# Optimization experiments

Hardware: AMD Instinct MI355X
Metric: run time of the kernel (lower is better)

The kernel has to match this reference:

```python
import jax, jax.numpy as jnp
import numpy as np

B, N, M, HA, HB, H = 16, 256, 12, 64, 64, 4
DIN = 2 * HA + HB
DOUT = 4 * H * HA


def _bn(x, g, b, eps=1e-5):
    # BatchNorm1d forward with batch statistics (training-mode math), x: [R, C]
    m = jnp.mean(x, axis=0)
    v = jnp.var(x, axis=0)
    return (x - m) * jax.lax.rsqrt(v + eps) * g + b


def setup_inputs() -> dict:
    key = jax.random.key(0)
    ks = jax.random.split(key, 6)
    atom_emb = jax.random.normal(ks[0], (B, N, HA), jnp.float32)
    nbr_emb = jax.random.normal(ks[1], (B, N, M, HB), jnp.float32)
    nbr_adj_list = jax.random.randint(ks[2], (B, N, M), 0, N)
    atom_mask = jnp.ones((B, N, 1), jnp.float32)
    W_full = jax.random.normal(ks[3], (DIN, DOUT), jnp.float32) / np.sqrt(DIN)
    b_full = jnp.zeros((DOUT,), jnp.float32)
    W_final = jax.random.normal(ks[4], (H * HA, HA), jnp.float32) / np.sqrt(H * HA)
    b_final = jnp.zeros((HA,), jnp.float32)
    bn1_g = jnp.ones((HA,), jnp.float32)
    bn1_b = jnp.zeros((HA,), jnp.float32)
    bn2_g = jnp.ones((HA,), jnp.float32)
    bn2_b = jnp.zeros((HA,), jnp.float32)
    return dict(atom_emb=atom_emb, nbr_emb=nbr_emb, atom_mask=atom_mask,
                W_full=W_full, b_full=b_full, W_final=W_final, b_final=b_final,
                bn1_g=bn1_g, bn1_b=bn1_b, bn2_g=bn2_g, bn2_b=bn2_b,
                nbr_adj_list=nbr_adj_list)


def reference(atom_emb, nbr_emb, atom_mask, W_full, b_full, W_final, b_final,
              bn1_g, bn1_b, bn2_g, bn2_b, nbr_adj_list):
    # Gather neighbor atom embeddings: [B,N,M,HA]
    bidx = jnp.arange(B)[:, None, None]
    atom_nbr = atom_emb[bidx, nbr_adj_list]
    atom_nbr = atom_nbr * atom_mask[..., None]  # mask [B,N,1,1]

    mask3 = jnp.broadcast_to(atom_mask, (B, N, M))  # [B,N,M]

    # Concat self, neighbor, bond embeddings -> [B,N,M,2HA+HB]
    self_emb = jnp.broadcast_to(atom_emb[:, :, None, :], (B, N, M, HA))
    total = jnp.concatenate([self_emb, atom_nbr, nbr_emb], axis=-1)

    tg = total @ W_full + b_full  # [B,N,M,4*H*HA]
    gate, core, a1, a2 = jnp.split(tg, 4, axis=-1)
    core = core.reshape(B, N, M, H, HA)
    a1 = a1.reshape(B, N, M, H, HA)
    a2 = a2.reshape(B, N, M, H, HA)

    # Masked multi-head attention over the neighbor dim (M x M per atom)
    bias = (1.0 - mask3)[:, :, None, None, :] * -10000.0  # [B,N,1,1,M]
    scores = jnp.einsum('bnmhd,bnkhd->bnhmk', a1, a2) / np.sqrt(H) + bias
    probs = jax.nn.softmax(scores, axis=-1)  # dropout is identity in eval
    ctx = jnp.einsum('bnhmk,bnkhd->bnmhd', probs, core)  # [B,N,M,H,HA]

    core = jax.nn.relu(ctx)
    gate = jax.nn.sigmoid(gate.reshape(B, N, M, H, HA))
    summed = (gate * core).reshape(B, N, M, H * HA) @ W_final + b_final  # [B,N,M,HA]

    summed = _bn(summed.reshape(-1, HA), bn1_g, bn1_b).reshape(B, N, M, HA)
    summed = jax.nn.relu(summed)
    summed = jnp.sum(summed, axis=2)  # reduce over neighbors -> [B,N,HA]
    summed = _bn(summed.reshape(-1, HA), bn2_g, bn2_b).reshape(B, N, HA)
    return jax.nn.relu(atom_emb + summed)
```

## Files before the change

### kernel.cpp

```cpp
#include <hip/hip_runtime.h>

#define BB   16
#define NN   256
#define MM   12
#define HAc  64
#define Hh   4

#define PLD  264
#define TGLD 521

typedef __attribute__((ext_vector_type(8))) short bf16x8;
typedef __attribute__((ext_vector_type(4))) float f32x4;

__device__ __forceinline__ unsigned short bf16_rne(float x) {
    unsigned u = __builtin_bit_cast(unsigned, x);
    unsigned r = u + 0x7fffu + ((u >> 16) & 1u);
    return (unsigned short)(r >> 16);
}
__device__ __forceinline__ float bf16f(unsigned short h) {
    unsigned u = ((unsigned)h) << 16;
    return __builtin_bit_cast(float, u);
}
__device__ __forceinline__ void split8(float4 a, float4 b, bf16x8& hi, bf16x8& lo) {
    float v[8] = {a.x, a.y, a.z, a.w, b.x, b.y, b.z, b.w};
    #pragma unroll
    for (int j = 0; j < 8; ++j) {
        unsigned short h = bf16_rne(v[j]);
        hi[j] = (short)h;
        lo[j] = (short)bf16_rne(v[j] - bf16f(h));
    }
}

__global__ __launch_bounds__(256) void k0a_pack(
    const float* __restrict__ W_full,
    const float* __restrict__ W_final,
    short* __restrict__ w12pk,
    short* __restrict__ w3pk,
    short* __restrict__ wfpk)
{
    const int t = threadIdx.x;
    if (blockIdx.x < 128) {
        const int gid  = blockIdx.x * 256 + t;
        const int lane = gid & 63;
        const int rest = gid >> 6;
        const int p  = rest & 1;
        const int ks = (rest >> 1) & 1;
        const int nt = rest >> 2;
        const int rbase = (nt >= 64 ? 64 : 0) + ks * 32 + (lane >> 4) * 8;
        const int n  = (nt & 63) * 16 + (lane & 15);
        bf16x8 o;
        #pragma unroll
        for (int j = 0; j < 8; ++j) {
            float v = W_full[(rbase + j) * 1024 + n];
            unsigned short h = bf16_rne(v);
            o[j] = p ? (short)bf16_rne(v - bf16f(h)) : (short)h;
        }
        *((bf16x8*)(w12pk + ((nt * 4 + ks * 2 + p) * 64 + lane) * 8)) = o;
    } else if (blockIdx.x < 192) {
        const int gid  = (blockIdx.x - 128) * 256 + t;
        const int lane = gid & 63;
        const int rest = gid >> 6;
        const int p  = rest & 1;
        const int ks = (rest >> 1) & 1;
        const int nt = rest >> 2;
        const int kb = ks * 32 + (lane >> 4) * 8;
        const int n  = nt * 16 + (lane & 15);
        bf16x8 o;
        #pragma unroll
        for (int j = 0; j < 8; ++j) {
            float v = W_full[(128 + kb + j) * 1024 + n];
            unsigned short h = bf16_rne(v);
            o[j] = p ? (short)bf16_rne(v - bf16f(h)) : (short)h;
        }
        *((bf16x8*)(w3pk + ((nt * 4 + ks * 2 + p) * 64 + lane) * 8)) = o;
    } else {
        const int idx  = (blockIdx.x - 192) * 256 + t;
        const int lane = idx & 63;
        const int rest = idx >> 6;
        const int p  = rest & 1;
        const int ks = (rest >> 1) & 7;
        const int nt = rest >> 4;
        const int kb = ks * 32 + (lane >> 4) * 8;
        const int n  = nt * 16 + (lane & 15);
        bf16x8 o;
        #pragma unroll
        for (int j = 0; j < 8; ++j) {
            float v = W_final[(kb + j) * 64 + n];
            unsigned short h = bf16_rne(v);
            o[j] = p ? (short)bf16_rne(v - bf16f(h)) : (short)h;
        }
        *((bf16x8*)(wfpk + ((nt * 8 + ks) * 2 + p) * 512 + lane * 8)) = o;
    }
}

__global__ __launch_bounds__(256) void k0b_p12(
    const float* __restrict__ atom_emb,
    const float* __restrict__ b_full,
    const short* __restrict__ w12pk,
    float* __restrict__ p1b,
    float* __restrict__ p2)
{
    const int r0   = blockIdx.x * 16;
    const int t    = threadIdx.x;
    const int w    = t >> 6;
    const int lane = t & 63;
    const int lr   = lane & 15;
    const int kg   = lane >> 4;

    bf16x8 aAh[2], aAl[2];
    #pragma unroll
    for (int ks = 0; ks < 2; ++ks) {
        const float4* ap = (const float4*)(atom_emb + (r0 + lr) * 64 + ks * 32 + kg * 8);
        split8(ap[0], ap[1], aAh[ks], aAl[ks]);
    }

    const bf16x8* W12P = (const bf16x8*)w12pk;
    #pragma unroll 4
    for (int i = 0; i < 32; ++i) {
        const int nt = w * 32 + i;
        bf16x8 Bh0 = W12P[(nt * 4 + 0) * 64 + lane];
        bf16x8 Bl0 = W12P[(nt * 4 + 1) * 64 + lane];
        bf16x8 Bh1 = W12P[(nt * 4 + 2) * 64 + lane];
        bf16x8 Bl1 = W12P[(nt * 4 + 3) * 64 + lane];
        const int n = (nt & 63) * 16 + lr;
        f32x4 acc;
        if (nt < 64) {
            float bv = b_full[n];
            acc[0] = bv; acc[1] = bv; acc[2] = bv; acc[3] = bv;
        } else {
            acc[0] = 0.f; acc[1] = 0.f; acc[2] = 0.f; acc[3] = 0.f;
        }
        acc = __builtin_amdgcn_mfma_f32_16x16x32_bf16(aAh[0], Bh0, acc, 0, 0, 0);
        acc = __builtin_amdgcn_mfma_f32_16x16x32_bf16(aAh[0], Bl0, acc, 0, 0, 0);
        acc = __builtin_amdgcn_mfma_f32_16x16x32_bf16(aAl[0], Bh0, acc, 0, 0, 0);
        acc = __builtin_amdgcn_mfma_f32_16x16x32_bf16(aAh[1], Bh1, acc, 0, 0, 0);
        acc = __builtin_amdgcn_mfma_f32_16x16x32_bf16(aAh[1], Bl1, acc, 0, 0, 0);
        acc = __builtin_amdgcn_mfma_f32_16x16x32_bf16(aAl[1], Bh1, acc, 0, 0, 0);
        float* dst = (nt < 64) ? p1b : p2;
        #pragma unroll
        for (int r = 0; r < 4; ++r)
            dst[(r0 + kg * 4 + r) * 1024 + n] = acc[r];
    }
}

__global__ __launch_bounds__(256) void k1_fused(
    const float* __restrict__ nbr_emb,
    const float* __restrict__ atom_mask,
    const float* __restrict__ p1b,
    const float* __restrict__ p2,
    const short* __restrict__ w3pk,
    const short* __restrict__ wfpk,
    const float* __restrict__ b_final,
    const int*   __restrict__ adj,
    float* __restrict__ pre)
{
    __shared__ __align__(16) float tg[12][TGLD];
    __shared__ __align__(16) short a1hi[12 * PLD];
    __shared__ __align__(16) short a1lo[12 * PLD];
    __shared__ __align__(16) short a2hi[12 * PLD];
    __shared__ __align__(16) short a2lo[12 * PLD];
    __shared__ float scr[Hh][MM][MM];

    const int bn   = blockIdx.x;
    const int b    = bn >> 8;
    const int t    = threadIdx.x;
    const int w    = t >> 6;
    const int lane = t & 63;
    const int lr   = lane & 15;
    const int kg   = lane >> 4;
    const float mask = atom_mask[bn];

    bf16x8 nAhi[2], nAlo[2];
    #pragma unroll
    for (int ks = 0; ks < 2; ++ks) {
        float4 v0 = make_float4(0.f, 0.f, 0.f, 0.f), v1 = v0;
        if (lr < 12) {
            const float4* np = (const float4*)(nbr_emb + bn * 768 + lr * 64 + ks * 32 + kg * 8);
            v0 = np[0]; v1 = np[1];
        }
        split8(v0, v1, nAhi[ks], nAlo[ks]);
    }

    int nr[4];
    #pragma unroll
    for (int r = 0; r < 4; ++r) {
        int m = kg * 4 + r;
        nr[r] = (m < 12) ? (b * NN + adj[bn * MM + m]) : 0;
    }

    {
        const bf16x8* W3P = (const bf16x8*)w3pk;
        #pragma unroll 4
        for (int i = 0; i < 16; ++i) {
            const int nt = w * 16 + i;
            const int n  = nt * 16 + lr;
            bf16x8 B0h = W3P[(nt * 4 + 0) * 64 + lane];
            bf16x8 B0l = W3P[(nt * 4 + 1) * 64 + lane];
            bf16x8 B1h = W3P[(nt * 4 + 2) * 64 + lane];
            bf16x8 B1l = W3P[(nt * 4 + 3) * 64 + lane];
            const float p1v = p1b[bn * 1024 + n];
            f32x4 acc;
            #pragma unroll
            for (int r = 0; r < 4; ++r) {
                float pv = (kg * 4 + r < 12) ? p2[nr[r] * 1024 + n] : 0.f;
                acc[r] = p1v + mask * pv;
            }
            acc = __builtin_amdgcn_mfma_f32_16x16x32_bf16(nAhi[0], B0h, acc, 0, 0, 0);
            acc = __builtin_amdgcn_mfma_f32_16x16x32_bf16(nAhi[0], B0l, acc, 0, 0, 0);
            acc = __builtin_amdgcn_mfma_f32_16x16x32_bf16(nAlo[0], B0h, acc, 0, 0, 0);
            acc = __builtin_amdgcn_mfma_f32_16x16x32_bf16(nAhi[1], B1h, acc, 0, 0, 0);
            acc = __builtin_amdgcn_mfma_f32_16x16x32_bf16(nAhi[1], B1l, acc, 0, 0, 0);
            acc = __builtin_amdgcn_mfma_f32_16x16x32_bf16(nAlo[1], B1h, acc, 0, 0, 0);
            if (kg < 3) {
                if (w < 2) {
                    #pragma unroll
                    for (int r = 0; r < 4; ++r) tg[kg * 4 + r][n] = acc[r];
                } else {
                    const int cl = i * 16 + lr;
                    short* phi = (w == 2) ? a1hi : a2hi;
                    short* plo = (w == 2) ? a1lo : a2lo;
                    #pragma unroll
                    for (int r = 0; r < 4; ++r) {
                        const int row = kg * 4 + r;
                        unsigned short h = bf16_rne(acc[r]);
                        phi[row * PLD + cl] = (short)h;
                        plo[row * PLD + cl] = (short)bf16_rne(acc[r] - bf16f(h));
                    }
                }
            }
        }
    }
    __syncthreads();

    {
        const int h = w;
        f32x4 sc = {0.f, 0.f, 0.f, 0.f};
        #pragma unroll
        for (int ks = 0; ks < 2; ++ks) {
            bf16x8 x1h = {0,0,0,0,0,0,0,0}, x1l = x1h, x2h = x1h, x2l = x1h;
            if (lr < 12) {
                const int col = h * 64 + ks * 32 + kg * 8;
                x1h = *(const bf16x8*)&a1hi[lr * PLD + col];
                x1l = *(const bf16x8*)&a1lo[lr * PLD + col];
                x2h = *(const bf16x8*)&a2hi[lr * PLD + col];
                x2l = *(const bf16x8*)&a2lo[lr * PLD + col];
            }
            sc = __builtin_amdgcn_mfma_f32_16x16x32_bf16(x1h, x2h, sc, 0, 0, 0);
            sc = __builtin_amdgcn_mfma_f32_16x16x32_bf16(x1h, x2l, sc, 0, 0, 0);
            sc = __builtin_amdgcn_mfma_f32_16x16x32_bf16(x1l, x2h, sc, 0, 0, 0);
        }
        const float bias = (1.0f - mask) * (-10000.0f);
        if (kg < 3 && lr < 12) {
            #pragma unroll
            for (int r = 0; r < 4; ++r)
                scr[h][kg * 4 + r][lr] = 0.5f * sc[r] + bias;
        }
    }
    __syncthreads();

    if (t < Hh * MM) {
        float* row = &scr[0][0][0] + t * MM;
        float mx = row[0];
        #pragma unroll
        for (int k = 1; k < MM; ++k) mx = fmaxf(mx, row[k]);
        float e[MM];
        float sum = 0.f;
        #pragma unroll
        for (int k = 0; k < MM; ++k) { e[k] = __expf(row[k] - mx); sum += e[k]; }
        float inv = 1.0f / sum;
        #pragma unroll
        for (int k = 0; k < MM; ++k) row[k] = e[k] * inv;
    }
    __syncthreads();

    {
        const int c = t;
        const int h = c >> 6;
        float cv[MM];
        #pragma unroll
        for (int k = 0; k < MM; ++k) cv[k] = tg[k][256 + c];
        #pragma unroll
        for (int m = 0; m < MM; ++m) {
            float s = 0.f;
            #pragma unroll
            for (int k = 0; k < MM; ++k) s += scr[h][m][k] * cv[k];
            float gv = tg[m][c];
            float gt = 1.0f / (1.0f + __expf(-gv));
            float gc = gt * fmaxf(s, 0.f);
            unsigned short hh = bf16_rne(gc);
            a1hi[m * PLD + c] = (short)hh;
            a1lo[m * PLD + c] = (short)bf16_rne(gc - bf16f(hh));
        }
    }
    __syncthreads();

    {
        const bf16x8* WFP = (const bf16x8*)wfpk;
        f32x4 acc = {0.f, 0.f, 0.f, 0.f};
        #pragma unroll 2
        for (int ks = 0; ks < 8; ++ks) {
            bf16x8 Ah = {0,0,0,0,0,0,0,0}, Al = Ah;
            if (lr < 12) {
                const int col = ks * 32 + kg * 8;
                Ah = *(const bf16x8*)&a1hi[lr * PLD + col];
                Al = *(const bf16x8*)&a1lo[lr * PLD + col];
            }
            bf16x8 Bh = WFP[(w * 8 + ks) * 128 + lane];
            bf16x8 Bl = WFP[(w * 8 + ks) * 128 + 64 + lane];
            acc = __builtin_amdgcn_mfma_f32_16x16x32_bf16(Ah, Bh, acc, 0, 0, 0);
            acc = __builtin_amdgcn_mfma_f32_16x16x32_bf16(Ah, Bl, acc, 0, 0, 0);
            acc = __builtin_amdgcn_mfma_f32_16x16x32_bf16(Al, Bh, acc, 0, 0, 0);
        }
        const int n = w * 16 + lr;
        const float bf = b_final[n];
        if (kg < 3) {
            #pragma unroll
            for (int r = 0; r < 4; ++r)
                pre[(bn * MM + kg * 4 + r) * HAc + n] = acc[r] + bf;
        }
    }
}

__global__ __launch_bounds__(256) void k2_stats1(const float* __restrict__ pre,
                                                 float* __restrict__ stats1)
{
    const int t  = threadIdx.x;
    const int j  = t & 63;
    const int rg = t >> 6;
    const int base = blockIdx.x * 192 + rg;
    float s = 0.f, q = 0.f;
    for (int i = 0; i < 48; ++i) {
        float v = pre[(base + i * 4) * HAc + j];
        s += v; q += v * v;
    }
    __shared__ float red[2][4][64];
    red[0][rg][j] = s;
    red[1][rg][j] = q;
    __syncthreads();
    if (t < 64) {
        float S = red[0][0][j] + red[0][1][j] + red[0][2][j] + red[0][3][j];
        float Q = red[1][0][j] + red[1][1][j] + red[1][2][j] + red[1][3][j];
        atomicAdd(&stats1[j], S);
        atomicAdd(&stats1[64 + j], Q);
    }
}

__global__ __launch_bounds__(256) void k3_bn1_sum(const float* __restrict__ pre,
                                                  const float* __restrict__ stats1,
                                                  const float* __restrict__ g1,
                                                  const float* __restrict__ b1,
                                                  float* __restrict__ tout,
                                                  float* __restrict__ stats2)
{
    const int t  = threadIdx.x;
    const int j  = t & 63;
    const int rg = t >> 6;
    const float invR = 1.0f / 49152.0f;
    const float mean = stats1[j] * invR;
    const float var  = stats1[64 + j] * invR - mean * mean;
    const float rstd = rsqrtf(var + 1e-5f);
    const float ga = g1[j], be = b1[j];

    float s2 = 0.f, q2 = 0.f;
    for (int i = 0; i < 4; ++i) {
        const int bnrow = blockIdx.x * 16 + rg + i * 4;
        float s = 0.f;
        #pragma unroll
        for (int m = 0; m < MM; ++m) {
            float x = pre[(bnrow * MM + m) * HAc + j];
            float y = (x - mean) * rstd * ga + be;
            s += fmaxf(y, 0.f);
        }
        tout[bnrow * HAc + j] = s;
        s2 += s; q2 += s * s;
    }
    __shared__ float red[2][4][64];
    red[0][rg][j] = s2;
    red[1][rg][j] = q2;
    __syncthreads();
    if (t < 64) {
        float S = red[0][0][j] + red[0][1][j] + red[0][2][j] + red[0][3][j];
        float Q = red[1][0][j] + red[1][1][j] + red[1][2][j] + red[1][3][j];
        atomicAdd(&stats2[j], S);
        atomicAdd(&stats2[64 + j], Q);
    }
}

__global__ __launch_bounds__(256) void k4_bn2_out(const float* __restrict__ tin,
                                                  const float* __restrict__ stats2,
                                                  const float* __restrict__ g2,
                                                  const float* __restrict__ b2,
                                                  const float* __restrict__ atom_emb,
                                                  float* __restrict__ out)
{
    const int i4 = blockIdx.x * 256 + threadIdx.x;
    const int j0 = (i4 & 15) * 4;
    const float invR = 1.0f / 4096.0f;
    float4 tv = ((const float4*)tin)[i4];
    float4 ae = ((const float4*)atom_emb)[i4];
    float4 r;
    {
        float mean = stats2[j0] * invR;
        float var  = stats2[64 + j0] * invR - mean * mean;
        r.x = fmaxf(ae.x + (tv.x - mean) * rsqrtf(var + 1e-5f) * g2[j0] + b2[j0], 0.f);
    }
    {
        float mean = stats2[j0 + 1] * invR;
        float var  = stats2[64 + j0 + 1] * invR - mean * mean;
        r.y = fmaxf(ae.y + (tv.y - mean) * rsqrtf(var + 1e-5f) * g2[j0 + 1] + b2[j0 + 1], 0.f);
    }
    {
        float mean = stats2[j0 + 2] * invR;
        float var  = stats2[64 + j0 + 2] * invR - mean * mean;
        r.z = fmaxf(ae.z + (tv.z - mean) * rsqrtf(var + 1e-5f) * g2[j0 + 2] + b2[j0 + 2], 0.f);
    }
    {
        float mean = stats2[j0 + 3] * invR;
        float var  = stats2[64 + j0 + 3] * invR - mean * mean;
        r.w = fmaxf(ae.w + (tv.w - mean) * rsqrtf(var + 1e-5f) * g2[j0 + 3] + b2[j0 + 3], 0.f);
    }
    ((float4*)out)[i4] = r;
}

extern "C" void kernel_launch(void* const* d_in, const int* in_sizes, int n_in,
                              void* d_out, int out_size, void* d_ws, size_t ws_size,
                              hipStream_t stream)
{
    const float* atom_emb = (const float*)d_in[0];
    const float* nbr_emb  = (const float*)d_in[1];
    const float* atom_msk = (const float*)d_in[2];
    const float* W_full   = (const float*)d_in[3];
    const float* b_full   = (const float*)d_in[4];
    const float* W_final  = (const float*)d_in[5];
    const float* b_final  = (const float*)d_in[6];
    const float* bn1_g    = (const float*)d_in[7];
    const float* bn1_b    = (const float*)d_in[8];
    const float* bn2_g    = (const float*)d_in[9];
    const float* bn2_b    = (const float*)d_in[10];
    const int*   adj      = (const int*)d_in[11];
    float* out = (float*)d_out;

    float* ws     = (float*)d_ws;
    float* stats1 = ws;
    float* stats2 = ws + 128;
    float* p1b    = ws + 256;
    float* p2     = p1b + 4194304;
    float* pre    = p2 + 4194304;
    short* w3pk   = (short*)(pre + 3145728);
    short* wfpk   = w3pk + 131072;
    short* w12pk  = wfpk + 32768;
    float* tout   = p1b;

    hipMemsetAsync(ws, 0, 256 * sizeof(float), stream);

    k0a_pack<<<208, 256, 0, stream>>>(W_full, W_final, w12pk, w3pk, wfpk);
    k0b_p12<<<256, 256, 0, stream>>>(atom_emb, b_full, w12pk, p1b, p2);
    k1_fused<<<BB * NN, 256, 0, stream>>>(nbr_emb, atom_msk, p1b, p2, w3pk, wfpk,
                                          b_final, adj, pre);
    k2_stats1<<<256, 256, 0, stream>>>(pre, stats1);
    k3_bn1_sum<<<256, 256, 0, stream>>>(pre, stats1, bn1_g, bn1_b, tout, stats2);
    k4_bn2_out<<<256, 256, 0, stream>>>(tout, stats2, bn2_g, bn2_b, atom_emb, out);
}
```

Baseline: 226.3 us.

## Fuse BN1 statistics into main kernel with binned atomics, drop memset

Computes the BN1 sum and sum-of-squares inside the fused kernel's epilogue using wave shuffles and atomics into 64 bins, which k3 then reduces. This removes the separate stats kernel and its re-read of the pre-BN buffer. The memset is folded into the pack kernel as extra zeroing blocks, and the p12 precompute grid is doubled so more blocks share the work. It also swaps the manual bf16 rounding for the library conversion and changes the score scratch indexing from h to w; these could alter numerics if the indices differ.

```diff
diff --git a/kernel.cpp b/kernel.cpp
--- a/kernel.cpp
+++ b/kernel.cpp
@@ -1,4 +1,5 @@
 #include <hip/hip_runtime.h>
+#include <hip/hip_bf16.h>
 
 #define BB   16
 #define NN   256
@@ -12,10 +13,8 @@
 typedef __attribute__((ext_vector_type(8))) short bf16x8;
 typedef __attribute__((ext_vector_type(4))) float f32x4;
 
-__device__ __forceinline__ unsigned short bf16_rne(float x) {
-    unsigned u = __builtin_bit_cast(unsigned, x);
-    unsigned r = u + 0x7fffu + ((u >> 16) & 1u);
-    return (unsigned short)(r >> 16);
+__device__ __forceinline__ unsigned short f2bf(float x) {
+    return __builtin_bit_cast(unsigned short, __float2bfloat16(x));
 }
 __device__ __forceinline__ float bf16f(unsigned short h) {
     unsigned u = ((unsigned)h) << 16;
@@ -25,9 +24,9 @@
     float v[8] = {a.x, a.y, a.z, a.w, b.x, b.y, b.z, b.w};
     #pragma unroll
     for (int j = 0; j < 8; ++j) {
-        unsigned short h = bf16_rne(v[j]);
+        unsigned short h = f2bf(v[j]);
         hi[j] = (short)h;
-        lo[j] = (short)bf16_rne(v[j] - bf16f(h));
+        lo[j] = (short)f2bf(v[j] - bf16f(h));
     }
 }
 
@@ -36,7 +35,8 @@
     const float* __restrict__ W_final,
     short* __restrict__ w12pk,
     short* __restrict__ w3pk,
-    short* __restrict__ wfpk)
+    short* __restrict__ wfpk,
+    float* __restrict__ zbase)
 {
     const int t = threadIdx.x;
     if (blockIdx.x < 128) {
@@ -52,8 +52,8 @@
         #pragma unroll
         for (int j = 0; j < 8; ++j) {
             float v = W_full[(rbase + j) * 1024 + n];
-            unsigned short h = bf16_rne(v);
-            o[j] = p ? (short)bf16_rne(v - bf16f(h)) : (short)h;
+            unsigned short h = f2bf(v);
+            o[j] = p ? (short)f2bf(v - bf16f(h)) : (short)h;
         }
         *((bf16x8*)(w12pk + ((nt * 4 + ks * 2 + p) * 64 + lane) * 8)) = o;
     } else if (blockIdx.x < 192) {
@@ -69,11 +69,11 @@
         #pragma unroll
         for (int j = 0; j < 8; ++j) {
             float v = W_full[(128 + kb + j) * 1024 + n];
-            unsigned short h = bf16_rne(v);
-            o[j] = p ? (short)bf16_rne(v - bf16f(h)) : (short)h;
+            unsigned short h = f2bf(v);
+            o[j] = p ? (short)f2bf(v - bf16f(h)) : (short)h;
         }
         *((bf16x8*)(w3pk + ((nt * 4 + ks * 2 + p) * 64 + lane) * 8)) = o;
-    } else {
+    } else if (blockIdx.x < 208) {
         const int idx  = (blockIdx.x - 192) * 256 + t;
         const int lane = idx & 63;
         const int rest = idx >> 6;
@@ -86,10 +86,13 @@
         #pragma unroll
         for (int j = 0; j < 8; ++j) {
             float v = W_final[(kb + j) * 64 + n];
-            unsigned short h = bf16_rne(v);
-            o[j] = p ? (short)bf16_rne(v - bf16f(h)) : (short)h;
+            unsigned short h = f2bf(v);
+            o[j] = p ? (short)f2bf(v - bf16f(h)) : (short)h;
         }
         *((bf16x8*)(wfpk + ((nt * 8 + ks) * 2 + p) * 512 + lane * 8)) = o;
+    } else {
+        const int gid = (blockIdx.x - 208) * 256 + t;
+        if (gid < 8320) zbase[gid] = 0.f;
     }
 }
 
@@ -116,8 +119,8 @@
 
     const bf16x8* W12P = (const bf16x8*)w12pk;
     #pragma unroll 4
-    for (int i = 0; i < 32; ++i) {
-        const int nt = w * 32 + i;
+    for (int i = 0; i < 16; ++i) {
+        const int nt = w * 32 + blockIdx.y * 16 + i;
         bf16x8 Bh0 = W12P[(nt * 4 + 0) * 64 + lane];
         bf16x8 Bl0 = W12P[(nt * 4 + 1) * 64 + lane];
         bf16x8 Bh1 = W12P[(nt * 4 + 2) * 64 + lane];
@@ -152,7 +155,8 @@
     const short* __restrict__ wfpk,
     const float* __restrict__ b_final,
     const int*   __restrict__ adj,
-    float* __restrict__ pre)
+    float* __restrict__ pre,
+    float* __restrict__ stats1b)
 {
     __shared__ __align__(16) float tg[12][TGLD];
     __shared__ __align__(16) short a1hi[12 * PLD];
@@ -222,9 +226,9 @@
                     #pragma unroll
                     for (int r = 0; r < 4; ++r) {
                         const int row = kg * 4 + r;
-                        unsigned short h = bf16_rne(acc[r]);
+                        unsigned short h = f2bf(acc[r]);
                         phi[row * PLD + cl] = (short)h;
-                        plo[row * PLD + cl] = (short)bf16_rne(acc[r] - bf16f(h));
+                        plo[row * PLD + cl] = (short)f2bf(acc[r] - bf16f(h));
                     }
                 }
             }
@@ -253,7 +257,7 @@
         if (kg < 3 && lr < 12) {
             #pragma unroll
             for (int r = 0; r < 4; ++r)
-                scr[h][kg * 4 + r][lr] = 0.5f * sc[r] + bias;
+                scr[w][kg * 4 + r][lr] = 0.5f * sc[r] + bias;
         }
     }
     __syncthreads();
@@ -287,9 +291,9 @@
             float gv = tg[m][c];
             float gt = 1.0f / (1.0f + __expf(-gv));
             float gc = gt * fmaxf(s, 0.f);
-            unsigned short hh = bf16_rne(gc);
+            unsigned short hh = f2bf(gc);
             a1hi[m * PLD + c] = (short)hh;
-            a1lo[m * PLD + c] = (short)bf16_rne(gc - bf16f(hh));
+            a1lo[m * PLD + c] = (short)f2bf(gc - bf16f(hh));
         }
     }
     __syncthreads();
@@ -313,40 +317,27 @@
         }
         const int n = w * 16 + lr;
         const float bf = b_final[n];
+        float ssum = 0.f, ssq = 0.f;
         if (kg < 3) {
             #pragma unroll
-            for (int r = 0; r < 4; ++r)
-                pre[(bn * MM + kg * 4 + r) * HAc + n] = acc[r] + bf;
-        }
-    }
-}
-
-__global__ __launch_bounds__(256) void k2_stats1(const float* __restrict__ pre,
-                                                 float* __restrict__ stats1)
-{
-    const int t  = threadIdx.x;
-    const int j  = t & 63;
-    const int rg = t >> 6;
-    const int base = blockIdx.x * 192 + rg;
-    float s = 0.f, q = 0.f;
-    for (int i = 0; i < 48; ++i) {
-        float v = pre[(base + i * 4) * HAc + j];
-        s += v; q += v * v;
-    }
-    __shared__ float red[2][4][64];
-    red[0][rg][j] = s;
-    red[1][rg][j] = q;
-    __syncthreads();
-    if (t < 64) {
-        float S = red[0][0][j] + red[0][1][j] + red[0][2][j] + red[0][3][j];
-        float Q = red[1][0][j] + red[1][1][j] + red[1][2][j] + red[1][3][j];
-        atomicAdd(&stats1[j], S);
-        atomicAdd(&stats1[64 + j], Q);
+            for (int r = 0; r < 4; ++r) {
+                float v = acc[r] + bf;
+                pre[(bn * MM + kg * 4 + r) * HAc + n] = v;
+                ssum += v; ssq += v * v;
+            }
+        }
+        ssum += __shfl_xor(ssum, 16); ssum += __shfl_xor(ssum, 32);
+        ssq  += __shfl_xor(ssq, 16);  ssq  += __shfl_xor(ssq, 32);
+        if (kg == 0) {
+            const int bin = bn & 63;
+            atomicAdd(&stats1b[bin * 128 + n], ssum);
+            atomicAdd(&stats1b[bin * 128 + 64 + n], ssq);
+        }
     }
 }
 
 __global__ __launch_bounds__(256) void k3_bn1_sum(const float* __restrict__ pre,
-                                                  const float* __restrict__ stats1,
+                                                  const float* __restrict__ stats1b,
                                                   const float* __restrict__ g1,
                                                   const float* __restrict__ b1,
                                                   float* __restrict__ tout,
@@ -355,9 +346,18 @@
     const int t  = threadIdx.x;
     const int j  = t & 63;
     const int rg = t >> 6;
+
+    __shared__ float sst[128];
+    if (t < 128) {
+        float s = 0.f;
+        for (int bin = 0; bin < 64; ++bin) s += stats1b[bin * 128 + t];
+        sst[t] = s;
+    }
+    __syncthreads();
+
     const float invR = 1.0f / 49152.0f;
-    const float mean = stats1[j] * invR;
-    const float var  = stats1[64 + j] * invR - mean * mean;
+    const float mean = sst[j] * invR;
+    const float var  = sst[64 + j] * invR - mean * mean;
     const float rstd = rsqrtf(var + 1e-5f);
     const float ga = g1[j], be = b1[j];
 
@@ -440,24 +440,21 @@
     const int*   adj      = (const int*)d_in[11];
     float* out = (float*)d_out;
 
-    float* ws     = (float*)d_ws;
-    float* stats1 = ws;
-    float* stats2 = ws + 128;
-    float* p1b    = ws + 256;
-    float* p2     = p1b + 4194304;
-    float* pre    = p2 + 4194304;
-    short* w3pk   = (short*)(pre + 3145728);
-    short* wfpk   = w3pk + 131072;
-    short* w12pk  = wfpk + 32768;
-    float* tout   = p1b;
-
-    hipMemsetAsync(ws, 0, 256 * sizeof(float), stream);
-
-    k0a_pack<<<208, 256, 0, stream>>>(W_full, W_final, w12pk, w3pk, wfpk);
-    k0b_p12<<<256, 256, 0, stream>>>(atom_emb, b_full, w12pk, p1b, p2);
+    float* ws      = (float*)d_ws;
+    float* stats2  = ws;
+    float* stats1b = ws + 128;
+    float* p1b     = ws + 8320;
+    float* p2      = p1b + 4194304;
+    float* pre     = p2 + 4194304;
+    short* w3pk    = (short*)(pre + 3145728);
+    short* wfpk    = w3pk + 131072;
+    short* w12pk   = wfpk + 32768;
+    float* tout    = p1b;
+
+    k0a_pack<<<241, 256, 0, stream>>>(W_full, W_final, w12pk, w3pk, wfpk, ws);
+    k0b_p12<<<dim3(256, 2), 256, 0, stream>>>(atom_emb, b_full, w12pk, p1b, p2);
     k1_fused<<<BB * NN, 256, 0, stream>>>(nbr_emb, atom_msk, p1b, p2, w3pk, wfpk,
-                                          b_final, adj, pre);
-    k2_stats1<<<256, 256, 0, stream>>>(pre, stats1);
-    k3_bn1_sum<<<256, 256, 0, stream>>>(pre, stats1, bn1_g, bn1_b, tout, stats2);
+                                          b_final, adj, pre, stats1b);
+    k3_bn1_sum<<<256, 256, 0, stream>>>(pre, stats1b, bn1_g, bn1_b, tout, stats2);
     k4_bn2_out<<<256, 256, 0, stream>>>(tout, stats2, bn2_g, bn2_b, atom_emb, out);
 }
```

Result: faster. 211.6 us (-6.5%).
